# Kernel optimization log

Measured on AMD Instinct MI355X. Metric: run time of the kernel, lower is better.

Reference implementation:

```python
import jax, jax.numpy as jnp
import numpy as np
import math

B, N, D, H = 4, 2048, 1024, 16
d = D // H
F = 2048                      # field_size
PAD = 8192                    # _next_fast_size(4*F) = 2^13
FB = PAD // 2 + 1             # rfft freq bins
NC = 32                       # spectral-gate control points
EPS = 1e-6                    # feature-map positivity floor


def setup_inputs():
    key = jax.random.key(0)
    ks = jax.random.split(key, 16)
    rn = lambda k, sh, s=0.02: (jax.random.normal(k, sh) * s).astype(jnp.float32)
    eye = jnp.eye(d, dtype=jnp.float32)
    n = jnp.arange(H, dtype=jnp.float32)
    return {
        "x": jax.random.normal(ks[0], (B, N, D), dtype=jnp.float32),
        "w_qkvg": rn(ks[1], (4 * D, D)),
        "b_qkvg": jnp.concatenate([jnp.zeros(3 * D), jnp.full((D,), 2.0)]).astype(jnp.float32),
        "w_out": rn(ks[2], (D, D)),
        "b_out": jnp.zeros((D,), jnp.float32),
        "qfm_w": jnp.stack([eye + rn(ks[3], (d, d)), eye + rn(ks[4], (d, d))]),
        "qfm_b": jnp.zeros((2, d), jnp.float32),
        "kfm_w": jnp.stack([eye + rn(ks[5], (d, d)), eye + rn(ks[6], (d, d))]),
        "kfm_b": jnp.zeros((2, d), jnp.float32),
        "wg_w": rn(ks[7], (1, d)),
        "wg_b": jnp.zeros((1,), jnp.float32),
        "ln_g": jnp.ones((d,), jnp.float32),
        "ln_b": jnp.zeros((d,), jnp.float32),
        "sg_w1": rn(ks[8], (D, D)),
        "sg_b1": jnp.zeros((D,), jnp.float32),
        "sg_w2": rn(ks[9], (H * NC, D), 0.001),
        "sg_b2": jnp.zeros((H * NC,), jnp.float32),
        "wave_freq": (math.pi * (2 * n + 1) / 2).astype(jnp.float32),
        "wave_damp": jnp.full((H,), -0.69, jnp.float32),
        "wave_phase": jnp.linspace(0.0, math.pi, H).astype(jnp.float32),
        "coupling": (jnp.eye(H, dtype=jnp.float32) + rn(ks[10], (H, H), 0.01)),
    }


def _featmap(x, w, b):
    # Hedgehog-style learned positive feature map: depth x (Linear -> ReLU), + eps
    for i in range(w.shape[0]):
        x = jax.nn.relu(x @ w[i].T + b[i])
    return x + EPS


def reference(x, w_qkvg, b_qkvg, w_out, b_out, qfm_w, qfm_b, kfm_w, kfm_b,
              wg_w, wg_b, ln_g, ln_b, sg_w1, sg_b1, sg_w2, sg_b2,
              wave_freq, wave_damp, wave_phase, coupling):
    # fused qkvg projection -> per-head tensors (B,H,N,d)
    qkvg = x @ w_qkvg.T + b_qkvg
    q, k, v, g = [t.reshape(B, N, H, d).transpose(0, 2, 1, 3)
                  for t in jnp.split(qkvg, 4, axis=-1)]
    phi_q = _featmap(q, qfm_w, qfm_b)
    phi_k = _featmap(k, kfm_w, kfm_b)
    wg = jax.nn.sigmoid(k @ wg_w.T + wg_b)  # (B,H,N,1) write gate

    # token -> field position mapping (cached buffers in the original)
    stride = (F - 1) / max(N - 1, 1)
    pos = jnp.clip(jnp.arange(N, dtype=jnp.float32) * stride, 0, F - 2)
    lo = jnp.clip(pos.astype(jnp.int32), 0, F - 2)
    hi = lo + 1
    frac = jnp.clip(pos - lo.astype(jnp.float32), 0.0, 1.0)

    # scatter numerator (gated phi_k*v) + denominator (gated phi_k) streams
    write = jnp.concatenate([wg * phi_k * v, wg * phi_k], axis=-1)  # (B,H,N,2d)
    field = jnp.zeros((B, H, F, 2 * d), jnp.float32)
    field = field.at[:, :, lo, :].add(write * (1.0 - frac)[:, None])
    field = field.at[:, :, hi, :].add(write * frac[:, None])

    # left-aligned causal damped-wave kernel per head
    t = jnp.arange(F, dtype=jnp.float32) / F
    kern = jnp.exp(-jnp.exp(wave_damp)[:, None] * t) * \
           jnp.cos(wave_freq[:, None] * t + wave_phase[:, None])  # (H,F)
    base_fft = jnp.fft.rfft(kern, n=PAD, axis=-1)                 # (H,FB) complex

    # content-adaptive spectral gate from token 0 (causally safe)
    q0 = q[:, :, 0, :]
    mu = q0.mean(-1, keepdims=True)
    var = q0.var(-1, keepdims=True)
    q0 = (q0 - mu) / jnp.sqrt(var + 1e-5) * ln_g + ln_b
    h1 = jax.nn.gelu(q0.reshape(B, H * d) @ sg_w1.T + sg_b1)
    ctrl = (h1 @ sg_w2.T + sg_b2).reshape(B, H, NC)
    ip = jnp.arange(FB, dtype=jnp.float32) * (NC - 1) / (FB - 1)  # align_corners=True
    il = jnp.clip(ip.astype(jnp.int32), 0, NC - 2)
    iw = ip - il.astype(jnp.float32)
    gate = ctrl[:, :, il] * (1.0 - iw) + ctrl[:, :, il + 1] * iw  # (B,H,FB)
    mod = base_fft[None] * (1.0 + gate)                           # (B,H,FB) complex

    # FFT-domain global convolution + head coupling
    conv = jnp.fft.irfft(jnp.fft.rfft(field, n=PAD, axis=2) * mod[..., None],
                         n=PAD, axis=2)[:, :, :F, :]
    conv = jnp.einsum('hg,bgfc->bhfc', coupling, conv)

    # linear-interp read-back at token positions
    y = conv[:, :, lo, :] * (1.0 - frac)[:, None] + conv[:, :, hi, :] * frac[:, None]
    y_num, y_den = y[..., :d], y[..., d:]
    den = jnp.abs(jnp.sum(phi_q * y_den, axis=-1, keepdims=True)) + 1e-4
    out_h = (phi_q * y_num / den) * jax.nn.sigmoid(g)
    return out_h.transpose(0, 2, 1, 3).reshape(B, N, D) @ w_out.T + b_out
```

## Files before the change

kernel.cpp:

```cpp
#include <hip/hip_runtime.h>
#include <math.h>

#define B_   4
#define N_   2048
#define D_   1024
#define H_   16
#define d_   64
#define F_   2048
#define PAD_ 8192
#define FB_  4097
#define NC_  32
#define EPS_ 1e-6f
#define PI_F 3.14159265358979323846f
#define PI_D 3.14159265358979323846

typedef unsigned short ushort_t;
typedef short bf16x8 __attribute__((ext_vector_type(8)));
typedef float f32x4  __attribute__((ext_vector_type(4)));

#define GLD16(gp, lp) __builtin_amdgcn_global_load_lds( \
    (const __attribute__((address_space(1))) unsigned int*)(const void*)(gp), \
    (__attribute__((address_space(3))) unsigned int*)(void*)(lp), 16, 0, 0)

__device__ __forceinline__ ushort_t bf16_rne(float v) {
    unsigned b = __float_as_uint(v);
    unsigned rb = b + 0x7fffu + ((b >> 16) & 1u);
    return (ushort_t)(rb >> 16);
}
__device__ __forceinline__ void split_bf16(float v, ushort_t& h, ushort_t& l) {
    h = bf16_rne(v);
    float fh = __uint_as_float((unsigned)h << 16);
    l = bf16_rne(v - fh);
}

__device__ __forceinline__ float2 cmul(float2 a, float2 w) {
    return make_float2(a.x * w.x - a.y * w.y, a.x * w.y + a.y * w.x);
}
__device__ __forceinline__ float2 cmulc(float2 a, float2 w) {
    return make_float2(a.x * w.x + a.y * w.y, a.y * w.x - a.x * w.y);
}

__global__ __launch_bounds__(256) void kern_twid(float2* __restrict__ twid,
                                                 float2* __restrict__ tw4,
                                                 const float* __restrict__ qfm_w,
                                                 const float* __restrict__ kfm_w,
                                                 float* __restrict__ Wt) {
    int idx = blockIdx.x * 256 + threadIdx.x;
    if (idx < 13 * 4096) {
        const int lh = idx >> 12, t = idx & 4095;
        const int hh = 1 << lh;
        const int j = t & (hh - 1);
        double s, c;
        sincos(-PI_D * (double)j / (double)hh, &s, &c);
        twid[idx] = make_float2((float)c, (float)s);
    } else {
        idx -= 13 * 4096;
        if (idx < 6 * 3072) {
            const int s = idx / 3072;
            const int r = idx - s * 3072;
            const int j = r / 3;
            const int m = r - 3 * j + 1;
            const int q = 1024 >> (2 * s);
            double sn, cs;
            sincos(-2.0 * PI_D * (double)(m * (j & (q - 1))) / (double)(4 * q), &sn, &cs);
            tw4[idx] = make_float2((float)cs, (float)sn);
        } else {
            idx -= 6 * 3072;
            if (idx < 4 * 4096) {
                const int mat = idx >> 12, e = idx & 4095;
                const int c = e >> 6, j = e & 63;
                const float* src = (mat < 2) ? qfm_w : kfm_w;
                const int l = mat & 1;
                Wt[mat * 4096 + c * 64 + j] = src[l * 4096 + j * 64 + c];
            }
        }
    }
}

__global__ __launch_bounds__(256) void kern_split3(
        const float* __restrict__ s0, ushort_t* __restrict__ h0, ushort_t* __restrict__ l0, int n0,
        const float* __restrict__ s1, ushort_t* __restrict__ h1, ushort_t* __restrict__ l1, int n1,
        const float* __restrict__ s2, ushort_t* __restrict__ h2, ushort_t* __restrict__ l2, int n2) {
    int i = blockIdx.x * 256 + threadIdx.x;
    const float* s; ushort_t* hh; ushort_t* ll; int k;
    if (i < n0)                { s = s0; hh = h0; ll = l0; k = i; }
    else if (i < n0 + n1)      { s = s1; hh = h1; ll = l1; k = i - n0; }
    else if (i < n0 + n1 + n2) { s = s2; hh = h2; ll = l2; k = i - n0 - n1; }
    else return;
    ushort_t h, l;
    split_bf16(s[k], h, l);
    hh[k] = h; ll[k] = l;
}

__global__ __launch_bounds__(256) void gemm_mfma(
        const ushort_t* __restrict__ Ah, const ushort_t* __restrict__ Al, int lda,
        const ushort_t* __restrict__ Bh, const ushort_t* __restrict__ Bl, int ldb,
        const float* __restrict__ bias, float* __restrict__ C,
        int Nn, int K) {
    __shared__ __align__(16) ushort_t At0[128 * 32];
    __shared__ __align__(16) ushort_t At1[128 * 32];
    __shared__ __align__(16) ushort_t Bt0[128 * 32];
    __shared__ __align__(16) ushort_t Bt1[128 * 32];

    const int tid = threadIdx.x;
    const int wv = tid >> 6, lane = tid & 63;
    const int quad = lane >> 4, lrow = lane & 15;
    const int m0 = blockIdx.y * 128, n0 = blockIdx.x * 128;
    const int mw = (wv >> 1) * 64, nw = (wv & 1) * 64;

    const int srow = lane >> 2;
    const int schunk = (((lane & 3) ^ ((lane >> 3) & 3)) * 8);
    const int qsw = ((quad ^ ((lrow >> 1) & 3)) * 8);

    f32x4 acc[4][4] = {};

    for (int k0 = 0; k0 < K; k0 += 32) {
        {
            const size_t ga = (size_t)(m0 + wv * 32 + srow) * lda + k0 + schunk;
            const size_t gb = (size_t)(n0 + wv * 32 + srow) * ldb + k0 + schunk;
            const size_t ga2 = ga + (size_t)16 * lda;
            const size_t gb2 = gb + (size_t)16 * ldb;
            GLD16(Ah + ga,  &At0[(wv * 32) * 32]);
            GLD16(Ah + ga2, &At0[(wv * 32 + 16) * 32]);
            GLD16(Al + ga,  &At1[(wv * 32) * 32]);
            GLD16(Al + ga2, &At1[(wv * 32 + 16) * 32]);
            GLD16(Bh + gb,  &Bt0[(wv * 32) * 32]);
            GLD16(Bh + gb2, &Bt0[(wv * 32 + 16) * 32]);
            GLD16(Bl + gb,  &Bt1[(wv * 32) * 32]);
            GLD16(Bl + gb2, &Bt1[(wv * 32 + 16) * 32]);
        }
        __syncthreads();

        bf16x8 a0[4], a1[4], b0[4], b1[4];
#pragma unroll
        for (int i = 0; i < 4; ++i) {
            a0[i] = *(const bf16x8*)&At0[(mw + i * 16 + lrow) * 32 + qsw];
            a1[i] = *(const bf16x8*)&At1[(mw + i * 16 + lrow) * 32 + qsw];
            b0[i] = *(const bf16x8*)&Bt0[(nw + i * 16 + lrow) * 32 + qsw];
            b1[i] = *(const bf16x8*)&Bt1[(nw + i * 16 + lrow) * 32 + qsw];
        }
#pragma unroll
        for (int mi = 0; mi < 4; ++mi)
#pragma unroll
            for (int nj = 0; nj < 4; ++nj) {
                acc[mi][nj] = __builtin_amdgcn_mfma_f32_16x16x32_bf16(a0[mi], b0[nj], acc[mi][nj], 0, 0, 0);
                acc[mi][nj] = __builtin_amdgcn_mfma_f32_16x16x32_bf16(a0[mi], b1[nj], acc[mi][nj], 0, 0, 0);
                acc[mi][nj] = __builtin_amdgcn_mfma_f32_16x16x32_bf16(a1[mi], b0[nj], acc[mi][nj], 0, 0, 0);
            }
        __syncthreads();
    }

#pragma unroll
    for (int mi = 0; mi < 4; ++mi) {
        const int row = m0 + mw + mi * 16 + quad * 4;
#pragma unroll
        for (int nj = 0; nj < 4; ++nj) {
            const int col = n0 + nw + nj * 16 + lrow;
            const float bv = bias[col];
#pragma unroll
            for (int r = 0; r < 4; ++r)
                C[(size_t)(row + r) * Nn + col] = acc[mi][nj][r] + bv;
        }
    }
}

__device__ __forceinline__ float gelu_f(float x) {
    return 0.5f * x * (1.f + tanhf(0.7978845608028654f * (x + 0.044715f * x * x * x)));
}

__global__ __launch_bounds__(256) void kern_gemv4(const float* __restrict__ A,
                                                  const float* __restrict__ W,
                                                  const float* __restrict__ bias,
                                                  float* __restrict__ C,
                                                  int Nn, int act) {
    const int tid = threadIdx.x;
    const int wv = tid >> 6, lane = tid & 63;
    const int col = blockIdx.x * 4 + wv;
    const float* wp = W + (size_t)col * D_;
    float a0 = 0.f, a1 = 0.f, a2 = 0.f, a3 = 0.f;
#pragma unroll
    for (int i = 0; i < 16; ++i) {
        int k = lane + i * 64;
        float w = wp[k];
        a0 += A[k] * w;
        a1 += A[D_ + k] * w;
        a2 += A[2 * D_ + k] * w;
        a3 += A[3 * D_ + k] * w;
    }
    for (int m = 1; m < 64; m <<= 1) {
        a0 += __shfl_xor(a0, m);
        a1 += __shfl_xor(a1, m);
        a2 += __shfl_xor(a2, m);
        a3 += __shfl_xor(a3, m);
    }
    if (lane == 0) {
        float bv = bias[col];
        float v0 = a0 + bv, v1 = a1 + bv, v2 = a2 + bv, v3 = a3 + bv;
        if (act) { v0 = gelu_f(v0); v1 = gelu_f(v1); v2 = gelu_f(v2); v3 = gelu_f(v3); }
        C[0 * Nn + col] = v0;
        C[1 * Nn + col] = v1;
        C[2 * Nn + col] = v2;
        C[3 * Nn + col] = v3;
    }
}

__global__ __launch_bounds__(256) void kern_feat(float* __restrict__ qkvg,
                                                 const float* __restrict__ Wt,
                                                 const float* __restrict__ qfm_b,
                                                 const float* __restrict__ kfm_b,
                                                 const float* __restrict__ wg_w,
                                                 const float* __restrict__ wg_b,
                                                 float* __restrict__ field) {
    __shared__ __align__(16) float in_t[64][68];
    __shared__ __align__(16) float tmp[64][68];
    __shared__ float wgbuf[64];

    const int tid = threadIdx.x;
    const int lane = tid & 63, grp = tid >> 6;
    const int n0 = blockIdx.x * 64;
    const int h = blockIdx.y, b = blockIdx.z;
    const size_t rowbase = (size_t)(b * N_ + n0) * 4096;

    const int lr4 = tid >> 4;
    const int lc4 = (tid & 15) * 4;

    const int rg = lane >> 4;
    const int cg4 = (lane & 15) * 4;
    const int rbase = grp * 16 + rg * 4;

#define LOAD64x64(dst, off) \
    for (int it = 0; it < 4; ++it) { \
        int r = lr4 + it * 16; \
        float4 v = *(const float4*)&qkvg[rowbase + (size_t)r * 4096 + (off) + lc4]; \
        *(float4*)&dst[r][lc4] = v; \
    }

#define MLP2_ACC(srcarr, Wg) \
    f32x4 acc[4] = {}; \
    for (int c4 = 0; c4 < 64; c4 += 4) { \
        f32x4 wv0 = *(const f32x4*)&(Wg)[(c4 + 0) * 64 + cg4]; \
        f32x4 wv1 = *(const f32x4*)&(Wg)[(c4 + 1) * 64 + cg4]; \
        f32x4 wv2 = *(const f32x4*)&(Wg)[(c4 + 2) * 64 + cg4]; \
        f32x4 wv3 = *(const f32x4*)&(Wg)[(c4 + 3) * 64 + cg4]; \
        _Pragma("unroll") for (int rr = 0; rr < 4; ++rr) { \
            f32x4 iv = *(const f32x4*)&srcarr[rbase + rr][c4]; \
            acc[rr] += wv0 * iv[0]; \
            acc[rr] += wv1 * iv[1]; \
            acc[rr] += wv2 * iv[2]; \
            acc[rr] += wv3 * iv[3]; \
        } \
    }

#define MLP2_STORE_LDS(dstarr, biasp, EPSV) { \
    f32x4 b4 = *(const f32x4*)&(biasp)[cg4]; \
    _Pragma("unroll") for (int rr = 0; rr < 4; ++rr) { \
        f32x4 v = acc[rr] + b4; \
        _Pragma("unroll") for (int k = 0; k < 4; ++k) v[k] = fmaxf(v[k], 0.f) + (EPSV); \
        *(f32x4*)&dstarr[rbase + rr][cg4] = v; } }

    LOAD64x64(in_t, D_ + h * 64)
    __syncthreads();
    if (tid < 64) {
        float s = 0.f;
        for (int c4 = 0; c4 < 64; c4 += 4) {
            float4 iv = *(const float4*)&in_t[tid][c4];
            s += iv.x * wg_w[c4] + iv.y * wg_w[c4 + 1] + iv.z * wg_w[c4 + 2] + iv.w * wg_w[c4 + 3];
        }
        s += wg_b[0];
        wgbuf[tid] = 1.f / (1.f + expf(-s));
    }
    {
        MLP2_ACC(in_t, Wt + 2 * 4096)
        MLP2_STORE_LDS(tmp, kfm_b, 0.f)
    }
    __syncthreads();
    {
        MLP2_ACC(tmp, Wt + 3 * 4096)
        MLP2_STORE_LDS(in_t, kfm_b + 64, EPS_)
    }
    __syncthreads();
    LOAD64x64(tmp, 2 * D_ + h * 64)
    __syncthreads();

    {
        float* frow = field + (size_t)(b * H_ + h) * 128 * F_;
        const bool last = (n0 == N_ - 64);
        for (int c = grp; c < 128; c += 4) {
            int i = lane;
            float v = (c < 64) ? wgbuf[i] * in_t[i][c] * tmp[i][c]
                               : wgbuf[i] * in_t[i][c - 64];
            if (last) {
                if (i == 62) {
                    float v2 = (c < 64) ? wgbuf[63] * in_t[63][c] * tmp[63][c]
                                        : wgbuf[63] * in_t[63][c - 64];
                    v += v2;
                } else if (i == 63) v = 0.f;
            }
            frow[(size_t)c * F_ + n0 + i] = v;
        }
    }
    __syncthreads();

    LOAD64x64(in_t, h * 64)
    __syncthreads();
    {
        MLP2_ACC(in_t, Wt)
        MLP2_STORE_LDS(tmp, qfm_b, 0.f)
    }
    __syncthreads();
    {
        MLP2_ACC(tmp, Wt + 4096)
        f32x4 b4 = *(const f32x4*)&qfm_b[64 + cg4];
#pragma unroll
        for (int rr = 0; rr < 4; ++rr) {
            f32x4 v = acc[rr] + b4;
#pragma unroll
            for (int k = 0; k < 4; ++k) v[k] = fmaxf(v[k], 0.f) + EPS_;
            *(f32x4*)&qkvg[rowbase + (size_t)(rbase + rr) * 4096 + D_ + h * 64 + cg4] = v;
        }
    }
#undef LOAD64x64
#undef MLP2_ACC
#undef MLP2_STORE_LDS
}

__global__ void kern_ln(const float* __restrict__ qkvg,
                        const float* __restrict__ ln_g,
                        const float* __restrict__ ln_b,
                        float* __restrict__ q0n) {
    const int bh = blockIdx.x, c = threadIdx.x;
    const int b = bh >> 4, h = bh & 15;
    float x = qkvg[(size_t)(b * N_) * 4096 + h * 64 + c];
    float mu = x;
    for (int m = 1; m < 64; m <<= 1) mu += __shfl_xor(mu, m);
    mu *= (1.f / 64.f);
    float dv = (x - mu) * (x - mu);
    for (int m = 1; m < 64; m <<= 1) dv += __shfl_xor(dv, m);
    float var = dv * (1.f / 64.f);
    q0n[b * 1024 + h * 64 + c] = (x - mu) * rsqrtf(var + 1e-5f) * ln_g[c] + ln_b[c];
}

template <int NT>
__device__ __forceinline__ void fft_fwd_dif_t(float* xr, float* xi, int tid, int logn,
                                              const float2* __restrict__ twid) {
    const int nb = 1 << (logn - 1);
    for (int lh = logn - 1; lh >= 0; --lh) {
        const int hh = 1 << lh;
        const float2* tws = twid + lh * 4096;
        for (int t = tid; t < nb; t += NT) {
            int j = t & (hh - 1);
            int i1 = ((t >> lh) << (lh + 1)) | j;
            int i2 = i1 + hh;
            float2 tw = tws[t];
            float ar = xr[i1], ai = xi[i1];
            float br = xr[i2], bi = xi[i2];
            xr[i1] = ar + br; xi[i1] = ai + bi;
            float tr = ar - br, ti = ai - bi;
            xr[i2] = tr * tw.x - ti * tw.y;
            xi[i2] = tr * tw.y + ti * tw.x;
        }
        __syncthreads();
    }
}

template <int NT>
__device__ __forceinline__ void fft_inv_dit_t(float* xr, float* xi, int tid, int logn,
                                              const float2* __restrict__ twid) {
    const int nb = 1 << (logn - 1);
    for (int lh = 0; lh < logn; ++lh) {
        const int hh = 1 << lh;
        const float2* tws = twid + lh * 4096;
        for (int t = tid; t < nb; t += NT) {
            int j = t & (hh - 1);
            int i1 = ((t >> lh) << (lh + 1)) | j;
            int i2 = i1 + hh;
            float2 tw = tws[t];
            float br = xr[i2], bi = xi[i2];
            float tr = br * tw.x + bi * tw.y;
            float ti = bi * tw.x - br * tw.y;
            float ar = xr[i1], ai = xi[i1];
            xr[i1] = ar + tr; xi[i1] = ai + ti;
            xr[i2] = ar - tr; xi[i2] = ai - ti;
        }
        __syncthreads();
    }
}

#define ZIDX(i) ((i) + ((i) >> 4))

template <int NT, int SBEG, int SEND>
__device__ __forceinline__ void fft4_fwd_stages(float2* z, int tid,
                                                const float2* __restrict__ tw4) {
#pragma unroll
    for (int s = SBEG; s < SEND; ++s) {
        const int q = 1024 >> (2 * s);
        const int qq = q + (q >> 4);
        const float2* tws = tw4 + s * 3072;
        for (int t = tid; t < 1024; t += NT) {
            int j = t & (q - 1);
            int base = ((t & ~(q - 1)) << 2) | j;
            int i0, i1, i2, i3;
            if (q >= 16) { i0 = ZIDX(base); i1 = i0 + qq; i2 = i1 + qq; i3 = i2 + qq; }
            else { i0 = ZIDX(base); i1 = ZIDX(base + q); i2 = ZIDX(base + 2 * q); i3 = ZIDX(base + 3 * q); }
            float2 a = z[i0], b = z[i1], c = z[i2], d = z[i3];
            float2 s0 = make_float2(a.x + c.x, a.y + c.y);
            float2 s1 = make_float2(a.x - c.x, a.y - c.y);
            float2 s2 = make_float2(b.x + d.x, b.y + d.y);
            float2 s3 = make_float2(b.x - d.x, b.y - d.y);
            float2 m1 = make_float2(s1.x + s3.y, s1.y - s3.x);
            float2 m2 = make_float2(s0.x - s2.x, s0.y - s2.y);
            float2 m3 = make_float2(s1.x - s3.y, s1.y + s3.x);
            z[i0] = make_float2(s0.x + s2.x, s0.y + s2.y);
            z[i1] = cmul(m1, tws[3 * j + 0]);
            z[i2] = cmul(m2, tws[3 * j + 1]);
            z[i3] = cmul(m3, tws[3 * j + 2]);
        }
        __syncthreads();
    }
}

__device__ __forceinline__ void bf4_fwd(float2& e0, float2& e1, float2& e2, float2& e3,
                                        const float2* __restrict__ tws, int j) {
    float2 a = e0, b = e1, c = e2, d = e3;
    float2 s0 = make_float2(a.x + c.x, a.y + c.y);
    float2 s1 = make_float2(a.x - c.x, a.y - c.y);
    float2 s2 = make_float2(b.x + d.x, b.y + d.y);
    float2 s3 = make_float2(b.x - d.x, b.y - d.y);
    float2 m1 = make_float2(s1.x + s3.y, s1.y - s3.x);
    float2 m2 = make_float2(s0.x - s2.x, s0.y - s2.y);
    float2 m3 = make_float2(s1.x - s3.y, s1.y + s3.x);
    e0 = make_float2(s0.x + s2.x, s0.y + s2.y);
    e1 = cmul(m1, tws[3 * j + 0]);
    e2 = cmul(m2, tws[3 * j + 1]);
    e3 = cmul(m3, tws[3 * j + 2]);
}
__device__ __forceinline__ void bf4_fwd_id(float2& e0, float2& e1, float2& e2, float2& e3) {
    float2 a = e0, b = e1, c = e2, d = e3;
    float2 s0 = make_float2(a.x + c.x, a.y + c.y);
    float2 s1 = make_float2(a.x - c.x, a.y - c.y);
    float2 s2 = make_float2(b.x + d.x, b.y + d.y);
    float2 s3 = make_float2(b.x - d.x, b.y - d.y);
    e0 = make_float2(s0.x + s2.x, s0.y + s2.y);
    e1 = make_float2(s1.x + s3.y, s1.y - s3.x);
    e2 = make_float2(s0.x - s2.x, s0.y - s2.y);
    e3 = make_float2(s1.x - s3.y, s1.y + s3.x);
}
__device__ __forceinline__ void bf4_inv(float2& e0, float2& e1, float2& e2, float2& e3,
                                        const float2* __restrict__ tws, int j) {
    float2 a = e0;
    float2 b = cmulc(e1, tws[3 * j + 0]);
    float2 c = cmulc(e2, tws[3 * j + 1]);
    float2 d = cmulc(e3, tws[3 * j + 2]);
    float2 p0 = make_float2(a.x + c.x, a.y + c.y);
    float2 p1 = make_float2(a.x - c.x, a.y - c.y);
    float2 p2 = make_float2(b.x + d.x, b.y + d.y);
    float2 p3 = make_float2(b.x - d.x, b.y - d.y);
    e0 = make_float2(p0.x + p2.x, p0.y + p2.y);
    e1 = make_float2(p1.x - p3.y, p1.y + p3.x);
    e2 = make_float2(p0.x - p2.x, p0.y - p2.y);
    e3 = make_float2(p1.x + p3.y, p1.y - p3.x);
}
__device__ __forceinline__ void bf4_inv_id(float2& e0, float2& e1, float2& e2, float2& e3) {
    float2 a = e0, b = e1, c = e2, d = e3;
    float2 p0 = make_float2(a.x + c.x, a.y + c.y);
    float2 p1 = make_float2(a.x - c.x, a.y - c.y);
    float2 p2 = make_float2(b.x + d.x, b.y + d.y);
    float2 p3 = make_float2(b.x - d.x, b.y - d.y);
    e0 = make_float2(p0.x + p2.x, p0.y + p2.y);
    e1 = make_float2(p1.x - p3.y, p1.y + p3.x);
    e2 = make_float2(p0.x - p2.x, p0.y - p2.y);
    e3 = make_float2(p1.x + p3.y, p1.y - p3.x);
}

__global__ __launch_bounds__(1024) void kern_prep(const float* __restrict__ freq,
                                                  const float* __restrict__ damp,
                                                  const float* __restrict__ phase,
                                                  const float* __restrict__ ctrl,
                                                  const float2* __restrict__ twid,
                                                  const float2* __restrict__ tw4,
                                                  float* __restrict__ GBR) {
    __shared__ float sm[2 * PAD_];
    float* xr = sm;
    float* xi = sm + PAD_;
    const int bh = blockIdx.x, tid = threadIdx.x;
    const int b = bh >> 4, h = bh & 15;

    const float fr = freq[h], ed = expf(damp[h]), ph = phase[h];
    for (int f = tid; f < PAD_; f += 1024) {
        float v = 0.f;
        if (f < F_) {
            float t = (float)f / (float)F_;
            v = expf(-ed * t) * cosf(fr * t + ph);
        }
        xr[f] = v; xi[f] = 0.f;
    }
    __syncthreads();
    fft_fwd_dif_t<1024>(xr, xi, tid, 13, twid);

    const float* cp = ctrl + b * (H_ * NC_) + h * NC_;
    for (int j = tid; j < PAD_; j += 1024) {
        int k = (int)(__brev((unsigned)j) >> 19);
        int kk = min(k, PAD_ - k);
        float ip = (float)kk * ((float)(NC_ - 1) / (float)(FB_ - 1));
        int il = min((int)ip, NC_ - 2);
        float iw = ip - (float)il;
        float m = 1.f + cp[il] * (1.f - iw) + cp[il + 1] * iw;
        xr[j] *= m;
        xi[j] *= m;
    }
    __syncthreads();
    fft_inv_dit_t<1024>(xr, xi, tid, 13, twid);

    float g[4];
    const float sc = 1.f / (float)PAD_;
#pragma unroll
    for (int u = 0; u < 4; ++u) {
        int j = tid + u * 1024;
        g[u] = ((j < 2048) ? xr[j] : xr[j + 4096]) * sc;
    }
    __syncthreads();
    float2* z = (float2*)sm;
#pragma unroll
    for (int u = 0; u < 4; ++u) {
        int j = tid + u * 1024;
        z[ZIDX(j)] = make_float2(g[u], 0.f);
    }
    __syncthreads();
    fft4_fwd_stages<1024, 0, 5>(z, tid, tw4);
    {
        const float sc2 = 1.f / 4096.f;
        const int t = tid;
        const int base = t << 2;
        float2 a = z[ZIDX(base)], bq = z[ZIDX(base + 1)];
        float2 c = z[ZIDX(base + 2)], dq = z[ZIDX(base + 3)];
        float2 s0 = make_float2(a.x + c.x, a.y + c.y);
        float2 s1 = make_float2(a.x - c.x, a.y - c.y);
        float2 s2 = make_float2(bq.x + dq.x, bq.y + dq.y);
        float2 s3 = make_float2(bq.x - dq.x, bq.y - dq.y);
        float2 o0 = make_float2(s0.x + s2.x, s0.y + s2.y);
        float2 o1 = make_float2(s1.x + s3.y, s1.y - s3.x);
        float2 o2 = make_float2(s0.x - s2.x, s0.y - s2.y);
        float2 o3 = make_float2(s1.x - s3.y, s1.y + s3.x);
        float2* Gp = (float2*)GBR + (size_t)bh * 4096 + base;
        Gp[0] = make_float2(o0.x * sc2, o0.y * sc2);
        Gp[1] = make_float2(o1.x * sc2, o1.y * sc2);
        Gp[2] = make_float2(o2.x * sc2, o2.y * sc2);
        Gp[3] = make_float2(o3.x * sc2, o3.y * sc2);
    }
}

#define LIDX(i) ((i) ^ (((i) >> 4) & 15))

__global__ __launch_bounds__(256) void kern_conv4(float* __restrict__ field,
                                                  const float* __restrict__ GBR,
                                                  const float2* __restrict__ tw4) {
    __shared__ float2 z[4096];
    const int tid = threadIdx.x;
    const int bh = blockIdx.x >> 6, cp = blockIdx.x & 63;
    float* rowx = field + ((size_t)bh * 128 + 2 * cp) * F_;
    float* rowy = rowx + F_;
    const float2* tws0 = tw4;
    const float2* tws1 = tw4 + 3072;
    const float2* tws2 = tw4 + 2 * 3072;
    const float2* tws3 = tw4 + 3 * 3072;
    const float2* tws4s = tw4 + 4 * 3072;

    float2 x[16];

    {
        const int j16 = tid;
#pragma unroll
        for (int m = 0; m < 8; ++m)
            x[m] = make_float2(rowx[j16 + 256 * m], rowy[j16 + 256 * m]);
#pragma unroll
        for (int m = 8; m < 16; ++m) x[m] = make_float2(0.f, 0.f);
#pragma unroll
        for (int r = 0; r < 4; ++r)
            bf4_fwd(x[r], x[r + 4], x[r + 8], x[r + 12], tws0, j16 + 256 * r);
#pragma unroll
        for (int c = 0; c < 4; ++c)
            bf4_fwd(x[4 * c], x[4 * c + 1], x[4 * c + 2], x[4 * c + 3], tws1, j16);
#pragma unroll
        for (int m = 0; m < 16; ++m) z[LIDX(j16 + 256 * m)] = x[m];
    }
    __syncthreads();

    {
        const int j16 = tid & 15;
        const int pb = (tid >> 4) * 256 + j16;
#pragma unroll
        for (int m = 0; m < 16; ++m) x[m] = z[LIDX(pb + 16 * m)];
#pragma unroll
        for (int r = 0; r < 4; ++r)
            bf4_fwd(x[r], x[r + 4], x[r + 8], x[r + 12], tws2, j16 + 16 * r);
#pragma unroll
        for (int c = 0; c < 4; ++c)
            bf4_fwd(x[4 * c], x[4 * c + 1], x[4 * c + 2], x[4 * c + 3], tws3, j16);
#pragma unroll
        for (int m = 0; m < 16; ++m) z[LIDX(pb + 16 * m)] = x[m];
    }
    __syncthreads();

    {
        const int pb = tid * 16;
#pragma unroll
        for (int m = 0; m < 16; ++m) x[m] = z[LIDX(pb + m)];
#pragma unroll
        for (int r = 0; r < 4; ++r)
            bf4_fwd(x[r], x[r + 4], x[r + 8], x[r + 12], tws4s, r);
#pragma unroll
        for (int c = 0; c < 4; ++c)
            bf4_fwd_id(x[4 * c], x[4 * c + 1], x[4 * c + 2], x[4 * c + 3]);
        const float2* G = (const float2*)GBR + (size_t)bh * 4096 + pb;
#pragma unroll
        for (int m = 0; m < 16; ++m) x[m] = cmul(x[m], G[m]);
#pragma unroll
        for (int c = 0; c < 4; ++c)
            bf4_inv_id(x[4 * c], x[4 * c + 1], x[4 * c + 2], x[4 * c + 3]);
#pragma unroll
        for (int r = 0; r < 4; ++r)
            bf4_inv(x[r], x[r + 4], x[r + 8], x[r + 12], tws4s, r);
#pragma unroll
        for (int m = 0; m < 16; ++m) z[LIDX(pb + m)] = x[m];
    }
    __syncthreads();

    {
        const int j16 = tid & 15;
        const int pb = (tid >> 4) * 256 + j16;
#pragma unroll
        for (int m = 0; m < 16; ++m) x[m] = z[LIDX(pb + 16 * m)];
#pragma unroll
        for (int c = 0; c < 4; ++c)
            bf4_inv(x[4 * c], x[4 * c + 1], x[4 * c + 2], x[4 * c + 3], tws3, j16);
#pragma unroll
        for (int r = 0; r < 4; ++r)
            bf4_inv(x[r], x[r + 4], x[r + 8], x[r + 12], tws2, j16 + 16 * r);
#pragma unroll
        for (int m = 0; m < 16; ++m) z[LIDX(pb + 16 * m)] = x[m];
    }
    __syncthreads();

    {
        const int j16 = tid;
#pragma unroll
        for (int m = 0; m < 16; ++m) x[m] = z[LIDX(j16 + 256 * m)];
#pragma unroll
        for (int c = 0; c < 4; ++c)
            bf4_inv(x[4 * c], x[4 * c + 1], x[4 * c + 2], x[4 * c + 3], tws1, j16);
#pragma unroll
        for (int r = 0; r < 4; ++r)
            bf4_inv(x[r], x[r + 4], x[r + 8], x[r + 12], tws0, j16 + 256 * r);
#pragma unroll
        for (int m = 0; m < 8; ++m) {
            rowx[j16 + 256 * m] = x[m].x;
            rowy[j16 + 256 * m] = x[m].y;
        }
    }
}

__global__ __launch_bounds__(1024) void kern_combine(float* __restrict__ qkvg,
                                                     const float* __restrict__ field,
                                                     const float* __restrict__ coupling) {
    __shared__ float cpl[16][16];
    __shared__ float sbuf[2][128][17];
    const int tid = threadIdx.x;
    if (tid < 256) cpl[tid >> 4][tid & 15] = coupling[tid];
    const int lane = tid & 63, wv = tid >> 6;
    const int n = blockIdx.x * 16 + wv;
    const int b = blockIdx.y;
    const int f0 = blockIdx.x * 16;
    const int fi = min(n, F_ - 2) - f0;
    const size_t row = (size_t)(b * N_ + n) * 4096;

    const int lc = tid >> 3, lk = (tid & 7) * 2;
    const float* fb = field + (size_t)b * 16 * 128 * F_;

    float2 rv = *(const float2*)&fb[(size_t)lc * F_ + f0 + lk];
    __syncthreads();
    sbuf[0][lc][lk] = rv.x; sbuf[0][lc][lk + 1] = rv.y;

    float ynum[16], yden[16];
#pragma unroll
    for (int hh = 0; hh < 16; ++hh) { ynum[hh] = 0.f; yden[hh] = 0.f; }

    for (int g = 0; g < 16; ++g) {
        if (g < 15)
            rv = *(const float2*)&fb[((size_t)(g + 1) * 128 + lc) * F_ + f0 + lk];
        __syncthreads();
        const float nv = sbuf[g & 1][lane][fi];
        const float dv = sbuf[g & 1][64 + lane][fi];
#pragma unroll
        for (int hh = 0; hh < 16; ++hh) {
            const float cg = cpl[hh][g];
            ynum[hh] += cg * nv;
            yden[hh] += cg * dv;
        }
        if (g < 15) { sbuf[(g + 1) & 1][lc][lk] = rv.x; sbuf[(g + 1) & 1][lc][lk + 1] = rv.y; }
    }

    ushort_t* rp = (ushort_t*)(qkvg + row);
#pragma unroll
    for (int hh = 0; hh < 16; ++hh) {
        float pq = qkvg[row + D_ + hh * 64 + lane];
        float gv = qkvg[row + 3 * D_ + hh * 64 + lane];
        float s = pq * yden[hh];
        for (int m = 1; m < 64; m <<= 1) s += __shfl_xor(s, m);
        float den = fabsf(s) + 1e-4f;
        float o = pq * ynum[hh] / den * (1.f / (1.f + expf(-gv)));
        ushort_t oh, ol;
        split_bf16(o, oh, ol);
        rp[hh * 64 + lane] = oh;
        rp[1024 + hh * 64 + lane] = ol;
    }
}

extern "C" void kernel_launch(void* const* d_in, const int* in_sizes, int n_in,
                              void* d_out, int out_size, void* d_ws, size_t ws_size,
                              hipStream_t stream) {
    const float* x      = (const float*)d_in[0];
    const float* w_qkvg = (const float*)d_in[1];
    const float* b_qkvg = (const float*)d_in[2];
    const float* w_out  = (const float*)d_in[3];
    const float* b_out  = (const float*)d_in[4];
    const float* qfm_w  = (const float*)d_in[5];
    const float* qfm_b  = (const float*)d_in[6];
    const float* kfm_w  = (const float*)d_in[7];
    const float* kfm_b  = (const float*)d_in[8];
    const float* wg_w   = (const float*)d_in[9];
    const float* wg_b   = (const float*)d_in[10];
    const float* ln_g   = (const float*)d_in[11];
    const float* ln_b   = (const float*)d_in[12];
    const float* sg_w1  = (const float*)d_in[13];
    const float* sg_b1  = (const float*)d_in[14];
    const float* sg_w2  = (const float*)d_in[15];
    const float* sg_b2  = (const float*)d_in[16];
    const float* wfreq  = (const float*)d_in[17];
    const float* wdamp  = (const float*)d_in[18];
    const float* wphase = (const float*)d_in[19];
    const float* coup   = (const float*)d_in[20];

    float* ws = (float*)d_ws;
    float*  qkvg   = ws;
    float*  field  = ws + 33554432;
    float*  GBR    = ws + 50593792;
    float2* twid   = (float2*)(ws + 51118080);
    float*  q0n    = ws + 51224576;
    float*  h1     = ws + 51228672;
    float*  ctrl   = ws + 51232768;
    ushort_t* wouth = (ushort_t*)(ws + 51234816);
    ushort_t* woutl = (ushort_t*)(ws + 51759104);
    float2* tw4    = (float2*)(ws + 52283392);
    float*  Wt     = ws + 52320256;

    ushort_t* xh  = (ushort_t*)(field);
    ushort_t* xl  = (ushort_t*)(field + 4194304);
    ushort_t* wqh = (ushort_t*)(field + 8388608);
    ushort_t* wql = (ushort_t*)(field + 10485760);

    kern_twid<<<(13 * 4096 + 6 * 3072 + 4 * 4096) / 256, 256, 0, stream>>>(
        twid, tw4, qfm_w, kfm_w, Wt);
    kern_split3<<<(B_ * N_ * D_ + 4 * D_ * D_ + D_ * D_) / 256, 256, 0, stream>>>(
        x, xh, xl, B_ * N_ * D_,
        w_qkvg, wqh, wql, 4 * D_ * D_,
        w_out, wouth, woutl, D_ * D_);

    for (int l = 0; l < 4; ++l) {
        const size_t aoff = (size_t)l * 2048 * D_;
        gemm_mfma<<<dim3(4096 / 128, 2048 / 128), 256, 0, stream>>>(
            xh + aoff, xl + aoff, D_, wqh, wql, D_, b_qkvg,
            qkvg + (size_t)l * 2048 * 4096, 4 * D_, D_);
    }

    kern_ln<<<B_ * H_, 64, 0, stream>>>(qkvg, ln_g, ln_b, q0n);
    kern_gemv4<<<D_ / 4, 256, 0, stream>>>(q0n, sg_w1, sg_b1, h1, D_, 1);
    kern_gemv4<<<(H_ * NC_) / 4, 256, 0, stream>>>(h1, sg_w2, sg_b2, ctrl, H_ * NC_, 0);

    kern_prep<<<B_ * H_, 1024, 0, stream>>>(wfreq, wdamp, wphase, ctrl, twid, tw4, GBR);

    kern_feat<<<dim3(N_ / 64, H_, B_), 256, 0, stream>>>(
        qkvg, Wt, qfm_b, kfm_b, wg_w, wg_b, field);

    kern_conv4<<<B_ * H_ * 64, 256, 0, stream>>>(field, GBR, tw4);

    kern_combine<<<dim3(N_ / 16, B_), 1024, 0, stream>>>(qkvg, field, coup);

    gemm_mfma<<<dim3(1024 / 128, 8192 / 128), 256, 0, stream>>>(
        (ushort_t*)qkvg, (ushort_t*)qkvg + 1024, 8192,
        wouth, woutl, D_, b_out, (float*)d_out, D_, D_);
}
```

Before: 690.5 us.

## Run feature-map MLPs on MFMA using three-way bf16 split emulation

The per-head 64x64 feature-map MLPs in kern_feat move from scalar FP32 FMA loops to bf16 MFMA instructions. Activations and weights are each split into three bf16 parts, and six cross products are accumulated to approximate FP32 precision. LDS tiles use XOR swizzling, and the weights are pre-split once in the setup kernel. The cost is extra split and pack work, more LDS traffic for the three planes, and some risk of small precision differences from the dropped low-order terms.

```diff
diff --git a/kernel.cpp b/kernel.cpp
--- a/kernel.cpp
+++ b/kernel.cpp
@@ -32,6 +32,14 @@
     float fh = __uint_as_float((unsigned)h << 16);
     l = bf16_rne(v - fh);
 }
+__device__ __forceinline__ void split3_bf16(float v, ushort_t& h, ushort_t& m, ushort_t& l) {
+    h = bf16_rne(v);
+    float fh = __uint_as_float((unsigned)h << 16);
+    float r = v - fh;
+    m = bf16_rne(r);
+    float fm = __uint_as_float((unsigned)m << 16);
+    l = bf16_rne(r - fm);
+}
 
 __device__ __forceinline__ float2 cmul(float2 a, float2 w) {
     return make_float2(a.x * w.x - a.y * w.y, a.x * w.y + a.y * w.x);
@@ -44,7 +52,9 @@
                                                  float2* __restrict__ tw4,
                                                  const float* __restrict__ qfm_w,
                                                  const float* __restrict__ kfm_w,
-                                                 float* __restrict__ Wt) {
+                                                 ushort_t* __restrict__ Wfh,
+                                                 ushort_t* __restrict__ Wfm,
+                                                 ushort_t* __restrict__ Wfl) {
     int idx = blockIdx.x * 256 + threadIdx.x;
     if (idx < 13 * 4096) {
         const int lh = idx >> 12, t = idx & 4095;
@@ -68,10 +78,13 @@
             idx -= 6 * 3072;
             if (idx < 4 * 4096) {
                 const int mat = idx >> 12, e = idx & 4095;
-                const int c = e >> 6, j = e & 63;
                 const float* src = (mat < 2) ? qfm_w : kfm_w;
-                const int l = mat & 1;
-                Wt[mat * 4096 + c * 64 + j] = src[l * 4096 + j * 64 + c];
+                float v = src[(mat & 1) * 4096 + e];
+                ushort_t hh, mm, ll;
+                split3_bf16(v, hh, mm, ll);
+                Wfh[mat * 4096 + e] = hh;
+                Wfm[mat * 4096 + e] = mm;
+                Wfl[mat * 4096 + e] = ll;
             }
         }
     }
@@ -204,19 +217,27 @@
     }
 }
 
+#define SWU(r, c) ((r) * 64 + ((((c) >> 3) ^ ((r) & 7)) << 3) + ((c) & 7))
+#define SWF(r, c) ((r) * 64 + ((c) ^ (((r) & 7) << 2)))
+
 __global__ __launch_bounds__(256) void kern_feat(float* __restrict__ qkvg,
-                                                 const float* __restrict__ Wt,
+                                                 const ushort_t* __restrict__ Wfh,
+                                                 const ushort_t* __restrict__ Wfm,
+                                                 const ushort_t* __restrict__ Wfl,
                                                  const float* __restrict__ qfm_b,
                                                  const float* __restrict__ kfm_b,
                                                  const float* __restrict__ wg_w,
                                                  const float* __restrict__ wg_b,
                                                  float* __restrict__ field) {
-    __shared__ __align__(16) float in_t[64][68];
-    __shared__ __align__(16) float tmp[64][68];
-    __shared__ float wgbuf[64];
+    __shared__ __align__(16) ushort_t bufA[3][64 * 64];
+    __shared__ __align__(16) ushort_t bufB[3][64 * 64];
+    float* bufAf = (float*)bufA;
+    float* bufBf = (float*)bufB;
 
     const int tid = threadIdx.x;
-    const int lane = tid & 63, grp = tid >> 6;
+    const int lane = tid & 63, wv = tid >> 6;
+    const int quad = lane >> 4, lrow = lane & 15;
+    const int mw = (wv >> 1) * 32, nw = (wv & 1) * 32;
     const int n0 = blockIdx.x * 64;
     const int h = blockIdx.y, b = blockIdx.z;
     const size_t rowbase = (size_t)(b * N_ + n0) * 4096;
@@ -224,75 +245,134 @@
     const int lr4 = tid >> 4;
     const int lc4 = (tid & 15) * 4;
 
-    const int rg = lane >> 4;
-    const int cg4 = (lane & 15) * 4;
-    const int rbase = grp * 16 + rg * 4;
-
-#define LOAD64x64(dst, off) \
+#define LOADSPLIT3(off, dst) \
     for (int it = 0; it < 4; ++it) { \
         int r = lr4 + it * 16; \
-        float4 v = *(const float4*)&qkvg[rowbase + (size_t)r * 4096 + (off) + lc4]; \
-        *(float4*)&dst[r][lc4] = v; \
-    }
-
-#define MLP2_ACC(srcarr, Wg) \
-    f32x4 acc[4] = {}; \
-    for (int c4 = 0; c4 < 64; c4 += 4) { \
-        f32x4 wv0 = *(const f32x4*)&(Wg)[(c4 + 0) * 64 + cg4]; \
-        f32x4 wv1 = *(const f32x4*)&(Wg)[(c4 + 1) * 64 + cg4]; \
-        f32x4 wv2 = *(const f32x4*)&(Wg)[(c4 + 2) * 64 + cg4]; \
-        f32x4 wv3 = *(const f32x4*)&(Wg)[(c4 + 3) * 64 + cg4]; \
-        _Pragma("unroll") for (int rr = 0; rr < 4; ++rr) { \
-            f32x4 iv = *(const f32x4*)&srcarr[rbase + rr][c4]; \
-            acc[rr] += wv0 * iv[0]; \
-            acc[rr] += wv1 * iv[1]; \
-            acc[rr] += wv2 * iv[2]; \
-            acc[rr] += wv3 * iv[3]; \
+        float4 v4 = *(const float4*)&qkvg[rowbase + (size_t)r * 4096 + (off) + lc4]; \
+        ushort_t h0, m0, l0, h1, m1, l1, h2, m2, l2, h3, m3, l3; \
+        split3_bf16(v4.x, h0, m0, l0); split3_bf16(v4.y, h1, m1, l1); \
+        split3_bf16(v4.z, h2, m2, l2); split3_bf16(v4.w, h3, m3, l3); \
+        int ix = SWU(r, lc4); \
+        *(uint2*)&(dst)[0][ix] = make_uint2((unsigned)h0 | ((unsigned)h1 << 16), \
+                                            (unsigned)h2 | ((unsigned)h3 << 16)); \
+        *(uint2*)&(dst)[1][ix] = make_uint2((unsigned)m0 | ((unsigned)m1 << 16), \
+                                            (unsigned)m2 | ((unsigned)m3 << 16)); \
+        *(uint2*)&(dst)[2][ix] = make_uint2((unsigned)l0 | ((unsigned)l1 << 16), \
+                                            (unsigned)l2 | ((unsigned)l3 << 16)); \
+    }
+
+#define MLP_MFMA3(src, wm, acc) \
+    _Pragma("unroll") for (int ks = 0; ks < 2; ++ks) { \
+        bf16x8 a0[2], a1[2], a2[2], b0[2], b1[2], b2[2]; \
+        _Pragma("unroll") for (int mt = 0; mt < 2; ++mt) { \
+            int ar = mw + mt * 16 + lrow; \
+            int ix = ar * 64 + (((ks * 4 + quad) ^ (ar & 7)) << 3); \
+            a0[mt] = *(const bf16x8*)&(src)[0][ix]; \
+            a1[mt] = *(const bf16x8*)&(src)[1][ix]; \
+            a2[mt] = *(const bf16x8*)&(src)[2][ix]; \
         } \
-    }
-
-#define MLP2_STORE_LDS(dstarr, biasp, EPSV) { \
-    f32x4 b4 = *(const f32x4*)&(biasp)[cg4]; \
-    _Pragma("unroll") for (int rr = 0; rr < 4; ++rr) { \
-        f32x4 v = acc[rr] + b4; \
-        _Pragma("unroll") for (int k = 0; k < 4; ++k) v[k] = fmaxf(v[k], 0.f) + (EPSV); \
-        *(f32x4*)&dstarr[rbase + rr][cg4] = v; } }
-
-    LOAD64x64(in_t, D_ + h * 64)
-    __syncthreads();
-    if (tid < 64) {
+        _Pragma("unroll") for (int nt = 0; nt < 2; ++nt) { \
+            int br = nw + nt * 16 + lrow; \
+            int ixw = (wm) * 4096 + br * 64 + ks * 32 + quad * 8; \
+            b0[nt] = *(const bf16x8*)&Wfh[ixw]; \
+            b1[nt] = *(const bf16x8*)&Wfm[ixw]; \
+            b2[nt] = *(const bf16x8*)&Wfl[ixw]; \
+        } \
+        _Pragma("unroll") for (int mt = 0; mt < 2; ++mt) \
+        _Pragma("unroll") for (int nt = 0; nt < 2; ++nt) { \
+            acc[mt][nt] = __builtin_amdgcn_mfma_f32_16x16x32_bf16(a0[mt], b0[nt], acc[mt][nt], 0, 0, 0); \
+            acc[mt][nt] = __builtin_amdgcn_mfma_f32_16x16x32_bf16(a0[mt], b1[nt], acc[mt][nt], 0, 0, 0); \
+            acc[mt][nt] = __builtin_amdgcn_mfma_f32_16x16x32_bf16(a1[mt], b0[nt], acc[mt][nt], 0, 0, 0); \
+            acc[mt][nt] = __builtin_amdgcn_mfma_f32_16x16x32_bf16(a0[mt], b2[nt], acc[mt][nt], 0, 0, 0); \
+            acc[mt][nt] = __builtin_amdgcn_mfma_f32_16x16x32_bf16(a1[mt], b1[nt], acc[mt][nt], 0, 0, 0); \
+            acc[mt][nt] = __builtin_amdgcn_mfma_f32_16x16x32_bf16(a2[mt], b0[nt], acc[mt][nt], 0, 0, 0); \
+        } \
+    }
+
+#define EPI_SPLIT3(acc, biasp, dst) \
+    _Pragma("unroll") for (int mt = 0; mt < 2; ++mt) \
+    _Pragma("unroll") for (int nt = 0; nt < 2; ++nt) { \
+        int col = nw + nt * 16 + lrow; \
+        float bv = (biasp)[col]; \
+        _Pragma("unroll") for (int r = 0; r < 4; ++r) { \
+            int row = mw + mt * 16 + quad * 4 + r; \
+            float v = fmaxf(acc[mt][nt][r] + bv, 0.f); \
+            ushort_t hh, mm, ll; split3_bf16(v, hh, mm, ll); \
+            int ix = SWU(row, col); \
+            (dst)[0][ix] = hh; (dst)[1][ix] = mm; (dst)[2][ix] = ll; \
+        } }
+
+    LOADSPLIT3(D_ + h * 64, bufA)
+    __syncthreads();
+
+    float wgv;
+    {
         float s = 0.f;
-        for (int c4 = 0; c4 < 64; c4 += 4) {
-            float4 iv = *(const float4*)&in_t[tid][c4];
-            s += iv.x * wg_w[c4] + iv.y * wg_w[c4 + 1] + iv.z * wg_w[c4 + 2] + iv.w * wg_w[c4 + 3];
+#pragma unroll
+        for (int c8 = 0; c8 < 8; ++c8) {
+            int ix = lane * 64 + ((c8 ^ (lane & 7)) << 3);
+#pragma unroll
+            for (int half = 0; half < 2; ++half) {
+                uint2 uh = *(const uint2*)&bufA[0][ix + half * 4];
+                uint2 um = *(const uint2*)&bufA[1][ix + half * 4];
+                uint2 ul = *(const uint2*)&bufA[2][ix + half * 4];
+                unsigned hw[4] = { uh.x & 0xffffu, uh.x >> 16, uh.y & 0xffffu, uh.y >> 16 };
+                unsigned mw_[4] = { um.x & 0xffffu, um.x >> 16, um.y & 0xffffu, um.y >> 16 };
+                unsigned lw[4] = { ul.x & 0xffffu, ul.x >> 16, ul.y & 0xffffu, ul.y >> 16 };
+#pragma unroll
+                for (int e = 0; e < 4; ++e) {
+                    float kv = __uint_as_float(hw[e] << 16) + __uint_as_float(mw_[e] << 16)
+                             + __uint_as_float(lw[e] << 16);
+                    s += kv * wg_w[c8 * 8 + half * 4 + e];
+                }
+            }
         }
         s += wg_b[0];
-        wgbuf[tid] = 1.f / (1.f + expf(-s));
-    }
-    {
-        MLP2_ACC(in_t, Wt + 2 * 4096)
-        MLP2_STORE_LDS(tmp, kfm_b, 0.f)
-    }
-    __syncthreads();
-    {
-        MLP2_ACC(tmp, Wt + 3 * 4096)
-        MLP2_STORE_LDS(in_t, kfm_b + 64, EPS_)
-    }
-    __syncthreads();
-    LOAD64x64(tmp, 2 * D_ + h * 64)
+        wgv = 1.f / (1.f + expf(-s));
+    }
+    float wg63 = __shfl(wgv, 63);
+
+    {
+        f32x4 acc[2][2] = {};
+        MLP_MFMA3(bufA, 2, acc)
+        EPI_SPLIT3(acc, kfm_b, bufB)
+    }
+    __syncthreads();
+    {
+        f32x4 acc[2][2] = {};
+        MLP_MFMA3(bufB, 3, acc)
+#pragma unroll
+        for (int mt = 0; mt < 2; ++mt)
+#pragma unroll
+        for (int nt = 0; nt < 2; ++nt) {
+            int col = nw + nt * 16 + lrow;
+            float bv = kfm_b[64 + col];
+#pragma unroll
+            for (int r = 0; r < 4; ++r) {
+                int row = mw + mt * 16 + quad * 4 + r;
+                bufAf[SWF(row, col)] = fmaxf(acc[mt][nt][r] + bv, 0.f) + EPS_;
+            }
+        }
+    }
+    __syncthreads();
+    for (int it = 0; it < 4; ++it) {
+        int r = lr4 + it * 16;
+        float4 v4 = *(const float4*)&qkvg[rowbase + (size_t)r * 4096 + 2 * D_ + h * 64 + lc4];
+        *(f32x4*)&bufBf[SWF(r, lc4)] = *(f32x4*)&v4;
+    }
     __syncthreads();
 
     {
         float* frow = field + (size_t)(b * H_ + h) * 128 * F_;
         const bool last = (n0 == N_ - 64);
-        for (int c = grp; c < 128; c += 4) {
+        for (int c = wv; c < 128; c += 4) {
             int i = lane;
-            float v = (c < 64) ? wgbuf[i] * in_t[i][c] * tmp[i][c]
-                               : wgbuf[i] * in_t[i][c - 64];
+            float v = (c < 64) ? wgv * bufAf[SWF(i, c)] * bufBf[SWF(i, c)]
+                               : wgv * bufAf[SWF(i, c - 64)];
             if (last) {
                 if (i == 62) {
-                    float v2 = (c < 64) ? wgbuf[63] * in_t[63][c] * tmp[63][c]
-                                        : wgbuf[63] * in_t[63][c - 64];
+                    float v2 = (c < 64) ? wg63 * bufAf[SWF(63, c)] * bufBf[SWF(63, c)]
+                                        : wg63 * bufAf[SWF(63, c - 64)];
                     v += v2;
                 } else if (i == 63) v = 0.f;
             }
@@ -301,27 +381,34 @@
     }
     __syncthreads();
 
-    LOAD64x64(in_t, h * 64)
-    __syncthreads();
-    {
-        MLP2_ACC(in_t, Wt)
-        MLP2_STORE_LDS(tmp, qfm_b, 0.f)
-    }
-    __syncthreads();
-    {
-        MLP2_ACC(tmp, Wt + 4096)
-        f32x4 b4 = *(const f32x4*)&qfm_b[64 + cg4];
-#pragma unroll
-        for (int rr = 0; rr < 4; ++rr) {
-            f32x4 v = acc[rr] + b4;
-#pragma unroll
-            for (int k = 0; k < 4; ++k) v[k] = fmaxf(v[k], 0.f) + EPS_;
-            *(f32x4*)&qkvg[rowbase + (size_t)(rbase + rr) * 4096 + D_ + h * 64 + cg4] = v;
-        }
-    }
-#undef LOAD64x64
-#undef MLP2_ACC
-#undef MLP2_STORE_LDS
+    LOADSPLIT3(h * 64, bufA)
+    __syncthreads();
+    {
+        f32x4 acc[2][2] = {};
+        MLP_MFMA3(bufA, 0, acc)
+        EPI_SPLIT3(acc, qfm_b, bufB)
+    }
+    __syncthreads();
+    {
+        f32x4 acc[2][2] = {};
+        MLP_MFMA3(bufB, 1, acc)
+#pragma unroll
+        for (int mt = 0; mt < 2; ++mt)
+#pragma unroll
+        for (int nt = 0; nt < 2; ++nt) {
+            int col = nw + nt * 16 + lrow;
+            float bv = qfm_b[64 + col];
+#pragma unroll
+            for (int r = 0; r < 4; ++r) {
+                int row = mw + mt * 16 + quad * 4 + r;
+                qkvg[rowbase + (size_t)row * 4096 + D_ + h * 64 + col] =
+                    fmaxf(acc[mt][nt][r] + bv, 0.f) + EPS_;
+            }
+        }
+    }
+#undef LOADSPLIT3
+#undef MLP_MFMA3
+#undef EPI_SPLIT3
 }
 
 __global__ void kern_ln(const float* __restrict__ qkvg,
@@ -751,7 +838,9 @@
     ushort_t* wouth = (ushort_t*)(ws + 51234816);
     ushort_t* woutl = (ushort_t*)(ws + 51759104);
     float2* tw4    = (float2*)(ws + 52283392);
-    float*  Wt     = ws + 52320256;
+    ushort_t* Wfh  = (ushort_t*)(ws + 52320256);
+    ushort_t* Wfm  = Wfh + 4 * 4096;
+    ushort_t* Wfl  = Wfm + 4 * 4096;
 
     ushort_t* xh  = (ushort_t*)(field);
     ushort_t* xl  = (ushort_t*)(field + 4194304);
@@ -759,7 +848,7 @@
     ushort_t* wql = (ushort_t*)(field + 10485760);
 
     kern_twid<<<(13 * 4096 + 6 * 3072 + 4 * 4096) / 256, 256, 0, stream>>>(
-        twid, tw4, qfm_w, kfm_w, Wt);
+        twid, tw4, qfm_w, kfm_w, Wfh, Wfm, Wfl);
     kern_split3<<<(B_ * N_ * D_ + 4 * D_ * D_ + D_ * D_) / 256, 256, 0, stream>>>(
         x, xh, xl, B_ * N_ * D_,
         w_qkvg, wqh, wql, 4 * D_ * D_,
@@ -779,7 +868,7 @@
     kern_prep<<<B_ * H_, 1024, 0, stream>>>(wfreq, wdamp, wphase, ctrl, twid, tw4, GBR);
 
     kern_feat<<<dim3(N_ / 64, H_, B_), 256, 0, stream>>>(
-        qkvg, Wt, qfm_b, kfm_b, wg_w, wg_b, field);
+        qkvg, Wfh, Wfm, Wfl, qfm_b, kfm_b, wg_w, wg_b, field);
 
     kern_conv4<<<B_ * H_ * 64, 256, 0, stream>>>(field, GBR, tw4);
 
```

Result: no change. 687.1 us (-0.5%).
